# Kernel optimization log

Measured on AMD Instinct MI355X. Metric: run time of the kernel, lower is better.

The kernel has to match this reference:

```python
import jax, jax.numpy as jnp
from jax import lax
import numpy as np

FEAT_W = 52      # feature map width/height
IMG_W = 210      # input image width/height
SUB = IMG_W // FEAT_W  # = 4, sub_sample stride
N_ANCHOR = 9
NMS_THRESH = 0.7
PRE_NMS = 12000
POST_NMS = 2000
MIN_SIZE = 16.0


def make_anchors():
    # Faithful vectorization of generateAnchors: outer loop over ctr_x, inner over ctr_y,
    # then c unpacked as (ctr_y, ctr_x) = (x_val, y_val); ratios outer, scales inner.
    vals = (np.arange(SUB, (FEAT_W + 1) * SUB, SUB) - SUB // 2).astype(np.float64)  # 2,6,...,210
    cy = np.repeat(vals, FEAT_W)   # outer loop value -> anchor ctr_y
    cx = np.tile(vals, FEAT_W)     # inner loop value -> anchor ctr_x
    ratios = np.array([0.5, 1.0, 2.0])
    scales = np.array([4.0, 8.0, 16.0])
    h = (SUB * scales[None, :] * np.sqrt(ratios[:, None])).reshape(-1)      # (9,)
    w = (SUB * scales[None, :] * np.sqrt(1.0 / ratios[:, None])).reshape(-1)
    a = np.stack([cy[:, None] - h / 2.0, cx[:, None] - w / 2.0,
                  cy[:, None] + h / 2.0, cx[:, None] + w / 2.0], axis=-1)   # (2704, 9, 4)
    return a.reshape(-1, 4).astype(np.float32)  # (24336, 4) as [y1,x1,y2,x2]

_ANCHORS = jnp.asarray(make_anchors())


def _conv(x, w, b):
    y = lax.conv_general_dilated(x, w, (1, 1), 'SAME',
                                 dimension_numbers=('NCHW', 'OIHW', 'NCHW'))
    return y + b[None, :, None, None]


def propose_regions(locs, obj):
    # locs: (1, 24336, 4); obj: (1, 24336)
    anc = _ANCHORS
    ah = anc[:, 2] - anc[:, 0]
    aw = anc[:, 3] - anc[:, 1]
    acy = anc[:, 0] + 0.5 * ah
    acx = anc[:, 1] + 0.5 * aw
    l = locs[0]
    s = obj[0]
    cy = l[:, 0] * ah + acy
    cx = l[:, 1] * aw + acx
    hh = jnp.exp(l[:, 2]) * ah
    ww = jnp.exp(l[:, 3]) * aw
    roi = jnp.stack([cy - 0.5 * hh, cx - 0.5 * ww,
                     cy + 0.5 * hh, cx + 0.5 * ww], axis=1)
    roi = jnp.clip(roi, 0.0, float(IMG_W))
    hs = roi[:, 2] - roi[:, 0]
    ws = roi[:, 3] - roi[:, 1]
    valid = (hs >= MIN_SIZE) & (ws >= MIN_SIZE)
    # min_size filter folded into score masking; invalid boxes start suppressed
    masked = jnp.where(valid, s, -jnp.inf)
    order = jnp.argsort(-masked)[:PRE_NMS]
    boxes = roi[order]          # (PRE_NMS, 4) sorted by descending score
    v = valid[order]
    sgb = lax.stop_gradient(boxes)
    areas = (sgb[:, 3] - sgb[:, 1] + 1.0) * (sgb[:, 2] - sgb[:, 0] + 1.0)
    idxs = jnp.arange(PRE_NMS)

    def body(supp, i):
        b = sgb[i]
        yy1 = jnp.maximum(b[0], sgb[:, 0])
        xx1 = jnp.maximum(b[1], sgb[:, 1])
        yy2 = jnp.minimum(b[2], sgb[:, 2])
        xx2 = jnp.minimum(b[3], sgb[:, 3])
        inter = jnp.maximum(0.0, xx2 - xx1 + 1.0) * jnp.maximum(0.0, yy2 - yy1 + 1.0)
        iou = inter / (areas[i] + areas - inter)
        new = supp | ((iou > NMS_THRESH) & (idxs > i))
        return jnp.where(supp[i], supp, new), None

    supp, _ = lax.scan(body, ~v, idxs)  # greedy sequential NMS, fixed length
    keep = ~supp
    rank = jnp.cumsum(keep.astype(jnp.int32)) - 1
    write = keep & (rank < POST_NMS)
    tgt = jnp.where(write, rank, POST_NMS)  # overflow/dropped rows go to scrap slot
    out = jnp.zeros((POST_NMS + 1, 4), boxes.dtype).at[tgt].set(
        jnp.where(write[:, None], boxes, 0.0))
    return out[:POST_NMS]  # (2000, 4), zero-padded


def _forward(x, conv1_w, conv1_b, reg_w, reg_b, cls_w, cls_b):
    h = _conv(x, conv1_w, conv1_b)        # (1,256,52,52), no activation (as in source)
    reg = _conv(h, reg_w, reg_b)          # (1,36,52,52)
    cls = _conv(h, cls_w, cls_b)          # (1,18,52,52)
    locs = jnp.transpose(reg, (0, 2, 3, 1)).reshape(1, -1, 4)          # (1,24336,4)
    cls_t = jnp.transpose(cls, (0, 2, 3, 1))                            # (1,52,52,18)
    obj = cls_t.reshape(1, FEAT_W, FEAT_W, N_ANCHOR, 2)[..., 1].reshape(1, -1)
    cls_scores = cls_t.reshape(1, -1, 2)                                # (1,24336,2)
    rois = propose_regions(locs, obj)
    return rois, locs, cls_scores, obj


def setup_inputs() -> dict:
    key = jax.random.key(0)
    ks = jax.random.split(key, 4)
    x = jax.random.normal(ks[0], (1, 256, FEAT_W, FEAT_W), jnp.float32)
    conv1_w = 0.01 * jax.random.normal(ks[1], (256, 256, 3, 3), jnp.float32)
    conv1_b = jnp.zeros((256,), jnp.float32)
    reg_w = 0.01 * jax.random.normal(ks[2], (N_ANCHOR * 4, 256, 1, 1), jnp.float32)
    reg_b = jnp.zeros((N_ANCHOR * 4,), jnp.float32)
    cls_w = 0.01 * jax.random.normal(ks[3], (N_ANCHOR * 2, 256, 1, 1), jnp.float32)
    cls_b = jnp.zeros((N_ANCHOR * 2,), jnp.float32)
    return {"x": x, "conv1_w": conv1_w, "conv1_b": conv1_b,
            "reg_w": reg_w, "reg_b": reg_b, "cls_w": cls_w, "cls_b": cls_b}


def reference(x, conv1_w, conv1_b, reg_w, reg_b, cls_w, cls_b):
    rois, locs, cls_scores, obj = _forward(x, conv1_w, conv1_b, reg_w, reg_b, cls_w, cls_b)
    return (rois, locs, cls_scores, obj, cls_scores)
```

## Files before the change

### kernel.cpp

```cpp
#include <hip/hip_runtime.h>

typedef unsigned long long u64;
typedef unsigned int u32;

#define FEAT 52
#define NPIX 2704
#define NANC 24336
#define PRE  12000
#define POST 2000
#define ROWW 192
#define PADW 54
#define PADS 2916

#define ROIS_OFF 0
#define LOCS_OFF 8000
#define CLS_OFF  105344
#define OBJ_OFF  154016
#define CLS2_OFF 178352

#define OFF_W64   0ull
#define OFF_H64   4718592ull
#define OFF_REG64 10256384ull
#define OFF_SC64  11035136ull
#define OFF_ROI64 11229824ull
#define OFF_KEYS  12008576ull
#define OFF_SBOX  12270720ull
#define OFF_SAREA 12663936ull
#define OFF_SUPP  12762240ull
#define OFF_MASK  12763776ull
#define OFF_XPAD  OFF_MASK
#define OFF_H64B  (OFF_MASK + 2985984ull)

__global__ __launch_bounds__(256) void k_prep(const float* __restrict__ x,
                                              float* __restrict__ xpad,
                                              const float* __restrict__ w,
                                              double* __restrict__ w64) {
    int b = blockIdx.x;
    if (b < 2916) {
        int t = b * 256 + threadIdx.x;
        int ci = t / PADS, pos = t % PADS;
        int iy = pos / PADW, ix = pos % PADW;
        float v = 0.f;
        if (iy >= 1 && iy <= 52 && ix >= 1 && ix <= 52)
            v = x[ci * NPIX + (iy - 1) * FEAT + (ix - 1)];
        xpad[t] = v;
    } else {
        int t = (b - 2916) * 256 + threadIdx.x;
        int j = t & 3;
        int r = t >> 2;
        int k = r % 9;
        int r2 = r / 9;
        int ci = r2 & 255;
        int g = r2 >> 8;
        w64[t] = (double)w[(((g * 4 + j) * 256) + ci) * 9 + k];
    }
}

__global__ __launch_bounds__(256) void k_conv3(const float* __restrict__ xpad,
                                               const double* __restrict__ w64,
                                               const float* __restrict__ b,
                                               double* __restrict__ h64,
                                               double* __restrict__ h64b) {
    const int p = blockIdx.x * 256 + threadIdx.x;
    const int o0 = blockIdx.y * 4;
    const int half = blockIdx.z;
    if (p >= NPIX) return;
    const int y = p / FEAT, xq = p % FEAT;
    double a0, a1, a2, a3;
    if (half == 0) {
        a0 = (double)b[o0+0]; a1 = (double)b[o0+1];
        a2 = (double)b[o0+2]; a3 = (double)b[o0+3];
    } else {
        a0 = a1 = a2 = a3 = 0.0;
    }
    const int c0 = half << 7;
    const float* xb = xpad + (size_t)c0 * PADS + y * PADW + xq;
    const double* wb = w64 + (size_t)blockIdx.y * 9216 + c0 * 36;
    #pragma unroll 2
    for (int ci = 0; ci < 128; ++ci) {
        float f0 = xb[0],   f1 = xb[1],   f2 = xb[2];
        float f3 = xb[54],  f4 = xb[55],  f5 = xb[56];
        float f6 = xb[108], f7 = xb[109], f8 = xb[110];
        double xv[9];
        xv[0]=(double)f0; xv[1]=(double)f1; xv[2]=(double)f2;
        xv[3]=(double)f3; xv[4]=(double)f4; xv[5]=(double)f5;
        xv[6]=(double)f6; xv[7]=(double)f7; xv[8]=(double)f8;
        const double* wr = wb + ci * 36;
        #pragma unroll
        for (int k = 0; k < 9; ++k) {
            a0 += xv[k] * wr[4*k+0];
            a1 += xv[k] * wr[4*k+1];
            a2 += xv[k] * wr[4*k+2];
            a3 += xv[k] * wr[4*k+3];
        }
        xb += PADS;
    }
    double* ho = (half == 0) ? h64 : h64b;
    ho[(o0+0)*NPIX + p] = a0;
    ho[(o0+1)*NPIX + p] = a1;
    ho[(o0+2)*NPIX + p] = a2;
    ho[(o0+3)*NPIX + p] = a3;
}

__global__ __launch_bounds__(64) void k_conv1(const double* __restrict__ h64,
                                              const double* __restrict__ h64b,
                                              const float* __restrict__ regw,
                                              const float* __restrict__ regb,
                                              const float* __restrict__ clsw,
                                              const float* __restrict__ clsb,
                                              float* __restrict__ out,
                                              double* __restrict__ reg64,
                                              double* __restrict__ score64) {
    const int g = blockIdx.y;
    const int p = blockIdx.x * 64 + threadIdx.x;
    if (p >= NPIX) return;
    const bool isreg = (g < 4);
    const float* wbase = isreg ? (regw + g * 9 * 256) : (clsw + (g - 4) * 9 * 256);
    const float* bbase = isreg ? (regb + g * 9)       : (clsb + (g - 4) * 9);
    double acc[9];
    #pragma unroll
    for (int j = 0; j < 9; ++j) acc[j] = (double)bbase[j];
    #pragma unroll 4
    for (int ci = 0; ci < 256; ++ci) {
        double h = h64[ci * NPIX + p] + h64b[ci * NPIX + p];
        #pragma unroll
        for (int j = 0; j < 9; ++j)
            acc[j] += h * (double)wbase[j * 256 + ci];
    }
    #pragma unroll
    for (int j = 0; j < 9; ++j) {
        int oc = g * 9 + j;
        float v = (float)acc[j];
        if (isreg) {
            out[LOCS_OFF + p*36 + oc] = v;
            reg64[p*36 + oc] = acc[j];
        } else {
            int c = oc - 36;
            out[CLS_OFF  + p*18 + c] = v;
            out[CLS2_OFF + p*18 + c] = v;
            if (c & 1) {
                out[OBJ_OFF + p*9 + (c >> 1)] = v;
                score64[p*9 + (c >> 1)] = acc[j];
            }
        }
    }
}

__global__ __launch_bounds__(256) void k_decode(const double* __restrict__ reg64,
                                                const double* __restrict__ score64,
                                                double* __restrict__ roi64,
                                                u64* __restrict__ keys) {
    int t = blockIdx.x * 256 + threadIdx.x;
    if (t >= NANC) { keys[t] = ~0ull; return; }
    int pos = t / 9, a = t % 9;
    int py = pos / FEAT, px = pos % FEAT;
    int ri = a / 3, si = a % 3;
    double rat = (ri == 0) ? 0.5 : (ri == 1 ? 1.0 : 2.0);
    double scl = (si == 0) ? 4.0 : (si == 1 ? 8.0 : 16.0);
    double hA = 4.0 * scl * sqrt(rat);
    double wA = 4.0 * scl * sqrt(1.0 / rat);
    double cy0 = 4.0 * py + 2.0, cx0 = 4.0 * px + 2.0;
    float y1f = (float)(cy0 - hA / 2.0), x1f = (float)(cx0 - wA / 2.0);
    float y2f = (float)(cy0 + hA / 2.0), x2f = (float)(cx0 + wA / 2.0);
    double ah = (double)y2f - (double)y1f, aw = (double)x2f - (double)x1f;
    double acy = (double)y1f + 0.5 * ah, acx = (double)x1f + 0.5 * aw;
    double l0 = reg64[4*t+0], l1 = reg64[4*t+1], l2 = reg64[4*t+2], l3 = reg64[4*t+3];
    double cy = l0 * ah + acy, cx = l1 * aw + acx;
    double hh = exp(l2) * ah,  ww = exp(l3) * aw;
    double r0 = fmin(fmax(cy - 0.5*hh, 0.0), 210.0);
    double r1 = fmin(fmax(cx - 0.5*ww, 0.0), 210.0);
    double r2 = fmin(fmax(cy + 0.5*hh, 0.0), 210.0);
    double r3 = fmin(fmax(cx + 0.5*ww, 0.0), 210.0);
    roi64[4*t+0] = r0; roi64[4*t+1] = r1; roi64[4*t+2] = r2; roi64[4*t+3] = r3;
    bool valid = (r2 - r0 >= 16.0) && (r3 - r1 >= 16.0);
    double m = valid ? score64[t] : -__builtin_huge_val();
    long long ll = __double_as_longlong(m);
    u64 u = (u64)ll;
    u64 mono = (ll < 0) ? ~u : (u ^ 0x8000000000000000ull);
    keys[t] = ((~mono) & 0xFFFFFFFFFFFF0000ull) | (u64)t;
}

__global__ __launch_bounds__(1024) void k_sortA(u64* __restrict__ keys) {
    __shared__ u64 s[8192];
    const int base = blockIdx.x * 8192;
    for (int t = threadIdx.x; t < 8192; t += 1024) s[t] = keys[base + t];
    __syncthreads();
    for (int k = 2; k <= 8192; k <<= 1) {
        for (int j = k >> 1; j > 0; j >>= 1) {
            for (int q = threadIdx.x; q < 4096; q += 1024) {
                int i = ((q & ~(j-1)) << 1) | (q & (j-1));
                int l = i | j;
                bool asc = (((base + i) & k) == 0);
                u64 A = s[i], B = s[l];
                bool sw = asc ? (A > B) : (A < B);
                if (sw) { s[i] = B; s[l] = A; }
            }
            __syncthreads();
        }
    }
    for (int t = threadIdx.x; t < 8192; t += 1024) keys[base + t] = s[t];
}

__global__ __launch_bounds__(1024) void k_sortB(u64* __restrict__ keys, int k) {
    __shared__ u64 s[8192];
    const int base = blockIdx.x * 8192;
    for (int t = threadIdx.x; t < 8192; t += 1024) s[t] = keys[base + t];
    __syncthreads();
    for (int j = 4096; j > 0; j >>= 1) {
        for (int q = threadIdx.x; q < 4096; q += 1024) {
            int i = ((q & ~(j-1)) << 1) | (q & (j-1));
            int l = i | j;
            bool asc = (((base + i) & k) == 0);
            u64 A = s[i], B = s[l];
            bool sw = asc ? (A > B) : (A < B);
            if (sw) { s[i] = B; s[l] = A; }
        }
        __syncthreads();
    }
    for (int t = threadIdx.x; t < 8192; t += 1024) keys[base + t] = s[t];
}

__global__ __launch_bounds__(256) void k_sortG(u64* __restrict__ keys, int k, int j) {
    int t = blockIdx.x * 256 + threadIdx.x;
    int i = ((t & ~(j-1)) << 1) | (t & (j-1));
    int l = i | j;
    bool asc = ((i & k) == 0);
    u64 A = keys[i], B = keys[l];
    bool sw = asc ? (A > B) : (A < B);
    if (sw) { keys[i] = B; keys[l] = A; }
}

__global__ __launch_bounds__(256) void k_gather(const u64* __restrict__ keys,
                                                const double* __restrict__ roi64,
                                                double* __restrict__ sbox,
                                                double* __restrict__ sarea,
                                                u64* __restrict__ suppinit) {
    int p = blockIdx.x * 256 + threadIdx.x;
    bool sup = true;
    if (p < PRE) {
        int idx = (int)(keys[p] & 0xFFFFull);
        double b0 = roi64[4*idx+0], b1 = roi64[4*idx+1];
        double b2 = roi64[4*idx+2], b3 = roi64[4*idx+3];
        sbox[4*p+0] = b0; sbox[4*p+1] = b1; sbox[4*p+2] = b2; sbox[4*p+3] = b3;
        sarea[p] = (b3 - b1 + 1.0) * (b2 - b0 + 1.0);
        sup = !((b2 - b0 >= 16.0) && (b3 - b1 >= 16.0));
    } else {
        sbox[4*p+0] = 0.0; sbox[4*p+1] = 0.0; sbox[4*p+2] = 0.0; sbox[4*p+3] = 0.0;
        sarea[p] = 1.0;
    }
    u64 ball = __ballot(sup);
    if ((threadIdx.x & 63) == 0) suppinit[p >> 6] = ball;
}

__global__ __launch_bounds__(256) void k_mask(const double* __restrict__ sbox,
                                              const double* __restrict__ sarea,
                                              u64* __restrict__ mask) {
    const int jt = blockIdx.x, it = blockIdx.y;
    const int ib = it * 64, jb0 = jt * 1024;
    if (jb0 + 1023 <= ib) {
        for (int t = threadIdx.x; t < 1024; t += 256) {
            int ti = t >> 4, w = t & 15;
            int i = ib + ti;
            if (i < PRE) mask[(size_t)i * ROWW + jt*16 + w] = 0ull;
        }
        return;
    }
    __shared__ double jbx[4112];
    __shared__ double jar[1040];
    for (int t = threadIdx.x; t < 4096; t += 256) jbx[t + (t >> 8)] = sbox[(size_t)jb0*4 + t];
    for (int t = threadIdx.x; t < 1024; t += 256) jar[t + (t >> 6)] = sarea[jb0 + t];
    __syncthreads();
    int ti = threadIdx.x >> 2;
    int i = ib + ti;
    if (i >= PRE) return;
    double iy1 = sbox[4*i+0], ix1 = sbox[4*i+1], iy2 = sbox[4*i+2], ix2 = sbox[4*i+3];
    double iar = sarea[i];
    for (int w = (threadIdx.x & 3); w < 16; w += 4) {
        const double* jb = &jbx[257 * w];
        const double* ja = &jar[65 * w];
        u64 bits = 0ull;
        int q0 = w * 64;
        for (int l = 0; l < 64; ++l) {
            double jy1 = jb[4*l+0], jx1 = jb[4*l+1], jy2 = jb[4*l+2], jx2 = jb[4*l+3];
            double yy1 = fmax(iy1, jy1), xx1 = fmax(ix1, jx1);
            double yy2 = fmin(iy2, jy2), xx2 = fmin(ix2, jx2);
            double iw = fmax(xx2 - xx1 + 1.0, 0.0);
            double ih = fmax(yy2 - yy1 + 1.0, 0.0);
            double inter = iw * ih;
            bool s = ((jb0 + q0 + l) > i) && (inter > 0.7 * (iar + ja[l] - inter));
            bits |= ((u64)s) << l;
        }
        mask[(size_t)i * ROWW + jt*16 + w] = bits;
    }
}

__device__ inline u64 rdl64(u64 v, int l) {
    u32 lo = (u32)__builtin_amdgcn_readlane((int)(u32)v, l);
    u32 hi = (u32)__builtin_amdgcn_readlane((int)(u32)(v >> 32), l);
    return ((u64)hi << 32) | (u64)lo;
}
#define RFL64(lo, hi) ( ((u64)(u32)__builtin_amdgcn_readfirstlane((int)(hi)) << 32) \
                      | (u64)(u32)__builtin_amdgcn_readfirstlane((int)(lo)) )

__global__ __launch_bounds__(512) void k_scan(const u64* __restrict__ mask,
                                              const u64* __restrict__ suppinit,
                                              const double* __restrict__ sbox,
                                              float* __restrict__ rois) {
    __shared__ u64 dbuf[2][4608];
    __shared__ u32 keptLDS[POST];
    __shared__ u32 supp8[2][16];
    __shared__ int rankS, doneS;
    const int tid = threadIdx.x;
    const u32* suppinit32 = (const u32*)suppinit;

    if (tid < 16)                 supp8[0][tid]      = suppinit32[tid];
    else if (tid < 32)            supp8[1][tid - 16] = suppinit32[tid];
    if (tid == 0) { rankS = 0; doneS = 0; }
    for (int q = tid; q < 4096; q += 512) {
        int r = q >> 3, w = q & 7;
        dbuf[0][r*9 + w] = (r < PRE) ? mask[(size_t)r * ROWW + w] : 0ull;
    }
    __syncthreads();

    int rank0 = 0;
    for (int c = 0; c < 24; ++c) {
        const int nc = c + 1;
        const int cb = c & 1, nb = nc & 1;
        if (tid < 64) {
            const int lane = tid;
            u64 i0 = RFL64(supp8[cb][0],  supp8[cb][1]);
            u64 i1 = RFL64(supp8[cb][2],  supp8[cb][3]);
            u64 i2 = RFL64(supp8[cb][4],  supp8[cb][5]);
            u64 i3 = RFL64(supp8[cb][6],  supp8[cb][7]);
            u64 i4 = RFL64(supp8[cb][8],  supp8[cb][9]);
            u64 i5 = RFL64(supp8[cb][10], supp8[cb][11]);
            u64 i6 = RFL64(supp8[cb][12], supp8[cb][13]);
            u64 i7 = RFL64(supp8[cb][14], supp8[cb][15]);
            u64 a0=0,a1=0,a2=0,a3=0,a4=0,a5=0,a6=0,a7=0;
            int rk = __builtin_amdgcn_readfirstlane(rankS);
            bool dn = false;
#define GROUP(G)                                                                \
            if (!dn) {                                                          \
                u64 z = ~(i##G | a##G);                                         \
                if (z) {                                                        \
                    u64 r0=0,r1=0,r2=0,r3=0,r4=0,r5=0,r6=0,r7=0;                \
                    if ((z >> lane) & 1ull) {                                   \
                        const u64* rowp = &dbuf[cb][(G*64 + lane)*9];           \
                        r0=rowp[0]; r1=rowp[1]; r2=rowp[2]; r3=rowp[3];         \
                        r4=rowp[4]; r5=rowp[5]; r6=rowp[6]; r7=rowp[7];         \
                    }                                                           \
                    u64 keptm = 0;                                              \
                    while (z) {                                                 \
                        int bpos = (int)__builtin_ctzll(z);                     \
                        u64 q0=rdl64(r0,bpos), q1=rdl64(r1,bpos);               \
                        u64 q2=rdl64(r2,bpos), q3=rdl64(r3,bpos);               \
                        u64 q4=rdl64(r4,bpos), q5=rdl64(r5,bpos);               \
                        u64 q6=rdl64(r6,bpos), q7=rdl64(r7,bpos);               \
                        keptm |= (1ull << bpos);                                \
                        z &= ~(1ull << bpos) & ~q##G;                           \
                        a0|=q0; a1|=q1; a2|=q2; a3|=q3;                         \
                        a4|=q4; a5|=q5; a6|=q6; a7|=q7;                         \
                    }                                                           \
                    int pc = __builtin_popcountll(keptm);                       \
                    int navail = POST - rk;                                     \
                    int mylot = __builtin_amdgcn_mbcnt_hi((u32)(keptm >> 32),   \
                                 __builtin_amdgcn_mbcnt_lo((u32)keptm, 0));     \
                    if (((keptm >> lane) & 1) && mylot < navail)                \
                        keptLDS[rk + mylot] = (u32)(c*512 + G*64 + lane);       \
                    if (pc >= navail) { rk = POST; dn = true; }                 \
                    else rk += pc;                                              \
                }                                                               \
            }
            GROUP(0) GROUP(1) GROUP(2) GROUP(3)
            GROUP(4) GROUP(5) GROUP(6) GROUP(7)
#undef GROUP
            if (lane == 0) { rankS = rk; if (dn) doneS = 1; }
        } else if (tid < 256) {
            if (nc < 24) {
                for (int q = tid - 64; q < 4096; q += 192) {
                    int r = q >> 3, w = q & 7;
                    int i = nc*512 + r;
                    dbuf[nb][r*9 + w] = (i < PRE) ? mask[(size_t)i * ROWW + nc*8 + w] : 0ull;
                }
            }
        } else {
            if (nc < 24 && rank0 > 0) {
                u64 acc[8] = {0,0,0,0,0,0,0,0};
                for (int k = tid - 256; k < rank0; k += 256) {
                    const u64* rp = mask + (size_t)keptLDS[k] * ROWW + nc*8;
                    #pragma unroll
                    for (int w = 0; w < 8; ++w) acc[w] |= rp[w];
                }
                #pragma unroll
                for (int w = 0; w < 8; ++w) {
                    u64 v = acc[w];
                    #pragma unroll
                    for (int s = 1; s < 64; s <<= 1)
                        v |= (u64)__shfl_xor((unsigned long long)v, s, 64);
                    if ((tid & 63) == 0) {
                        if ((u32)v)         atomicOr(&supp8[nb][2*w],   (u32)v);
                        if ((u32)(v >> 32)) atomicOr(&supp8[nb][2*w+1], (u32)(v >> 32));
                    }
                }
            }
        }
        __syncthreads();
        if (doneS) break;
        if (nc >= 24) break;
        const int rk1 = rankS;
        {
            int w = tid & 7;
            u64 acc = 0;
            for (int k = rank0 + (tid >> 3); k < rk1; k += 64)
                acc |= mask[(size_t)keptLDS[k] * ROWW + nc*8 + w];
            if ((u32)acc)         atomicOr(&supp8[nb][2*w],   (u32)acc);
            if ((u32)(acc >> 32)) atomicOr(&supp8[nb][2*w+1], (u32)(acc >> 32));
            if (tid < 16) supp8[cb][tid] = (c + 2 < 24) ? suppinit32[(c+2)*16 + tid] : 0u;
        }
        rank0 = rk1;
        __syncthreads();
    }
    __syncthreads();
    const int R = rankS;
    for (int r = tid; r < POST; r += 512) {
        if (r < R) {
            int p = (int)keptLDS[r];
            rois[4*r+0] = (float)sbox[4*p+0];
            rois[4*r+1] = (float)sbox[4*p+1];
            rois[4*r+2] = (float)sbox[4*p+2];
            rois[4*r+3] = (float)sbox[4*p+3];
        }
    }
}

extern "C" void kernel_launch(void* const* d_in, const int* in_sizes, int n_in,
                              void* d_out, int out_size, void* d_ws, size_t ws_size,
                              hipStream_t stream) {
    const float* x    = (const float*)d_in[0];
    const float* w1   = (const float*)d_in[1];
    const float* b1   = (const float*)d_in[2];
    const float* regw = (const float*)d_in[3];
    const float* regb = (const float*)d_in[4];
    const float* clsw = (const float*)d_in[5];
    const float* clsb = (const float*)d_in[6];
    float* out = (float*)d_out;

    char* ws = (char*)d_ws;
    double* w64    = (double*)(ws + OFF_W64);
    double* h64    = (double*)(ws + OFF_H64);
    double* reg64  = (double*)(ws + OFF_REG64);
    double* sc64   = (double*)(ws + OFF_SC64);
    double* roi64  = (double*)(ws + OFF_ROI64);
    u64*    keys   = (u64*)   (ws + OFF_KEYS);
    double* sbox   = (double*)(ws + OFF_SBOX);
    double* sarea  = (double*)(ws + OFF_SAREA);
    u64*    supp0  = (u64*)   (ws + OFF_SUPP);
    u64*    maskp  = (u64*)   (ws + OFF_MASK);
    float*  xpad   = (float*) (ws + OFF_XPAD);
    double* h64b   = (double*)(ws + OFF_H64B);

    (void)hipMemsetAsync(d_out, 0, 8000 * sizeof(float), stream);

    k_prep<<<5220, 256, 0, stream>>>(x, xpad, w1, w64);
    k_conv3<<<dim3(11, 64, 2), 256, 0, stream>>>(xpad, w64, b1, h64, h64b);
    k_conv1<<<dim3(43, 6), 64, 0, stream>>>(h64, h64b, regw, regb, clsw, clsb, out, reg64, sc64);
    k_decode<<<128, 256, 0, stream>>>(reg64, sc64, roi64, keys);

    k_sortA<<<4, 1024, 0, stream>>>(keys);
    k_sortG<<<64, 256, 0, stream>>>(keys, 16384, 8192);
    k_sortB<<<4, 1024, 0, stream>>>(keys, 16384);
    k_sortG<<<64, 256, 0, stream>>>(keys, 32768, 16384);
    k_sortG<<<64, 256, 0, stream>>>(keys, 32768, 8192);
    k_sortB<<<4, 1024, 0, stream>>>(keys, 32768);

    k_gather<<<48, 256, 0, stream>>>(keys, roi64, sbox, sarea, supp0);
    k_mask<<<dim3(12, 188), 256, 0, stream>>>(sbox, sarea, maskp);
    k_scan<<<1, 512, 0, stream>>>(maskp, supp0, sbox, out + ROIS_OFF);
}
```

Measured before the change: 590.5 us.

## Store NMS mask chunks bit-transposed in LDS and scan with ballots

The serial NMS scan wave now keeps a per-lane suppression bit vector. Each 512-row mask chunk is bit-transposed (64x64 transpose through xor shuffles) before it is written to LDS. The greedy loop then uses ballots over a per-lane flag instead of eight 64-bit readlanes per kept box, which shortens the serial critical path. In exchange, every chunk load pays for a shuffle-based transpose, and the helper waves are reorganised so all seven non-scan waves both prefetch/transpose and OR kept rows.

```diff
diff --git a/kernel.cpp b/kernel.cpp
--- a/kernel.cpp
+++ b/kernel.cpp
@@ -294,31 +294,55 @@
     }
 }
 
-__device__ inline u64 rdl64(u64 v, int l) {
-    u32 lo = (u32)__builtin_amdgcn_readlane((int)(u32)v, l);
-    u32 hi = (u32)__builtin_amdgcn_readlane((int)(u32)(v >> 32), l);
-    return ((u64)hi << 32) | (u64)lo;
-}
-#define RFL64(lo, hi) ( ((u64)(u32)__builtin_amdgcn_readfirstlane((int)(hi)) << 32) \
-                      | (u64)(u32)__builtin_amdgcn_readfirstlane((int)(lo)) )
+__device__ inline u64 shflx64(u64 v, int m) {
+    int lo = __shfl_xor((int)(u32)v, m, 64);
+    int hi = __shfl_xor((int)(u32)(v >> 32), m, 64);
+    return ((u64)(u32)hi << 32) | (u64)(u32)lo;
+}
+__device__ inline u64 bitT64(u64 x, int lane) {
+#define TS(d, Mlo) { u64 y = shflx64(x, d); \
+    x = (lane & d) ? ((x & ~(Mlo)) | ((y >> d) & (Mlo))) \
+                   : ((x & (Mlo))  | ((y & (Mlo)) << d)); }
+    TS(32, 0x00000000FFFFFFFFull)
+    TS(16, 0x0000FFFF0000FFFFull)
+    TS(8,  0x00FF00FF00FF00FFull)
+    TS(4,  0x0F0F0F0F0F0F0F0Full)
+    TS(2,  0x3333333333333333ull)
+    TS(1,  0x5555555555555555ull)
+#undef TS
+    return x;
+}
 
 __global__ __launch_bounds__(512) void k_scan(const u64* __restrict__ mask,
                                               const u64* __restrict__ suppinit,
                                               const double* __restrict__ sbox,
                                               float* __restrict__ rois) {
-    __shared__ u64 dbuf[2][4608];
+    __shared__ u64 dbufT[2][4096];
     __shared__ u32 keptLDS[POST];
     __shared__ u32 supp8[2][16];
     __shared__ int rankS, doneS;
     const int tid = threadIdx.x;
     const u32* suppinit32 = (const u32*)suppinit;
 
-    if (tid < 16)                 supp8[0][tid]      = suppinit32[tid];
-    else if (tid < 32)            supp8[1][tid - 16] = suppinit32[tid];
+    if (tid < 16)      supp8[0][tid]      = suppinit32[tid];
+    else if (tid < 32) supp8[1][tid - 16] = suppinit32[tid];
     if (tid == 0) { rankS = 0; doneS = 0; }
-    for (int q = tid; q < 4096; q += 512) {
-        int r = q >> 3, w = q & 7;
-        dbuf[0][r*9 + w] = (r < PRE) ? mask[(size_t)r * ROWW + w] : 0ull;
+    {
+        const int w = tid >> 6, lane = tid & 63;
+        const int g = w;
+        int row = g*64 + lane;
+        u64 rw[8];
+        if (row < PRE) {
+            const u64* rp = mask + (size_t)row * ROWW;
+            #pragma unroll
+            for (int h = 0; h < 8; ++h) rw[h] = rp[h];
+        } else {
+            #pragma unroll
+            for (int h = 0; h < 8; ++h) rw[h] = 0ull;
+        }
+        #pragma unroll
+        for (int h = 0; h < 8; ++h)
+            dbufT[0][(g*8 + h)*64 + lane] = bitT64(rw[h], lane);
     }
     __syncthreads();
 
@@ -328,78 +352,73 @@
         const int cb = c & 1, nb = nc & 1;
         if (tid < 64) {
             const int lane = tid;
-            u64 i0 = RFL64(supp8[cb][0],  supp8[cb][1]);
-            u64 i1 = RFL64(supp8[cb][2],  supp8[cb][3]);
-            u64 i2 = RFL64(supp8[cb][4],  supp8[cb][5]);
-            u64 i3 = RFL64(supp8[cb][6],  supp8[cb][7]);
-            u64 i4 = RFL64(supp8[cb][8],  supp8[cb][9]);
-            u64 i5 = RFL64(supp8[cb][10], supp8[cb][11]);
-            u64 i6 = RFL64(supp8[cb][12], supp8[cb][13]);
-            u64 i7 = RFL64(supp8[cb][14], supp8[cb][15]);
-            u64 a0=0,a1=0,a2=0,a3=0,a4=0,a5=0,a6=0,a7=0;
-            int rk = __builtin_amdgcn_readfirstlane(rankS);
+            u32 sup = 0;
+            #pragma unroll
+            for (int h = 0; h < 8; ++h)
+                sup |= ((supp8[cb][2*h + (lane >> 5)] >> (lane & 31)) & 1u) << h;
+            int rk = rankS;
             bool dn = false;
-#define GROUP(G)                                                                \
-            if (!dn) {                                                          \
-                u64 z = ~(i##G | a##G);                                         \
-                if (z) {                                                        \
-                    u64 r0=0,r1=0,r2=0,r3=0,r4=0,r5=0,r6=0,r7=0;                \
-                    if ((z >> lane) & 1ull) {                                   \
-                        const u64* rowp = &dbuf[cb][(G*64 + lane)*9];           \
-                        r0=rowp[0]; r1=rowp[1]; r2=rowp[2]; r3=rowp[3];         \
-                        r4=rowp[4]; r5=rowp[5]; r6=rowp[6]; r7=rowp[7];         \
-                    }                                                           \
-                    u64 keptm = 0;                                              \
-                    while (z) {                                                 \
-                        int bpos = (int)__builtin_ctzll(z);                     \
-                        u64 q0=rdl64(r0,bpos), q1=rdl64(r1,bpos);               \
-                        u64 q2=rdl64(r2,bpos), q3=rdl64(r3,bpos);               \
-                        u64 q4=rdl64(r4,bpos), q5=rdl64(r5,bpos);               \
-                        u64 q6=rdl64(r6,bpos), q7=rdl64(r7,bpos);               \
-                        keptm |= (1ull << bpos);                                \
-                        z &= ~(1ull << bpos) & ~q##G;                           \
-                        a0|=q0; a1|=q1; a2|=q2; a3|=q3;                         \
-                        a4|=q4; a5|=q5; a6|=q6; a7|=q7;                         \
-                    }                                                           \
-                    int pc = __builtin_popcountll(keptm);                       \
-                    int navail = POST - rk;                                     \
-                    int mylot = __builtin_amdgcn_mbcnt_hi((u32)(keptm >> 32),   \
-                                 __builtin_amdgcn_mbcnt_lo((u32)keptm, 0));     \
-                    if (((keptm >> lane) & 1) && mylot < navail)                \
-                        keptLDS[rk + mylot] = (u32)(c*512 + G*64 + lane);       \
-                    if (pc >= navail) { rk = POST; dn = true; }                 \
-                    else rk += pc;                                              \
-                }                                                               \
+            for (int g = 0; g < 8; ++g) {
+                bool agj = !((sup >> g) & 1u);
+                u64 z = __ballot(agj);
+                if (!z) continue;
+                u64 tg[8];
+                #pragma unroll
+                for (int h = 0; h < 8; ++h) tg[h] = dbufT[cb][(g*8 + h)*64 + lane];
+                u64 keptm = 0;
+                while (z) {
+                    int i = (int)__builtin_ctzll(z);
+                    keptm |= (1ull << i);
+                    agj = agj && !((tg[g] >> i) & 1ull);
+                    u64 m2 = (i < 63) ? (~0ull << (i + 1)) : 0ull;
+                    z = __ballot(agj) & m2;
+                }
+                int pc = __builtin_popcountll(keptm);
+                int navail = POST - rk;
+                int mylot = __builtin_amdgcn_mbcnt_hi((u32)(keptm >> 32),
+                             __builtin_amdgcn_mbcnt_lo((u32)keptm, 0));
+                if (((keptm >> lane) & 1) && mylot < navail)
+                    keptLDS[rk + mylot] = (u32)(c*512 + g*64 + lane);
+                if (pc >= navail) { rk = POST; dn = true; break; }
+                rk += pc;
+                #pragma unroll
+                for (int h = 0; h < 8; ++h)
+                    if (h > g && (tg[h] & keptm)) sup |= (1u << h);
             }
-            GROUP(0) GROUP(1) GROUP(2) GROUP(3)
-            GROUP(4) GROUP(5) GROUP(6) GROUP(7)
-#undef GROUP
             if (lane == 0) { rankS = rk; if (dn) doneS = 1; }
-        } else if (tid < 256) {
-            if (nc < 24) {
-                for (int q = tid - 64; q < 4096; q += 192) {
-                    int r = q >> 3, w = q & 7;
-                    int i = nc*512 + r;
-                    dbuf[nb][r*9 + w] = (i < PRE) ? mask[(size_t)i * ROWW + nc*8 + w] : 0ull;
+        } else if (nc < 24) {
+            const int w = tid >> 6, lane = tid & 63;
+            for (int g = w - 1; g < 8; g += 7) {
+                int row = nc*512 + g*64 + lane;
+                u64 rw[8];
+                if (row < PRE) {
+                    const u64* rp = mask + (size_t)row * ROWW + nc*8;
+                    #pragma unroll
+                    for (int h = 0; h < 8; ++h) rw[h] = rp[h];
+                } else {
+                    #pragma unroll
+                    for (int h = 0; h < 8; ++h) rw[h] = 0ull;
                 }
+                #pragma unroll
+                for (int h = 0; h < 8; ++h)
+                    dbufT[nb][(g*8 + h)*64 + lane] = bitT64(rw[h], lane);
             }
-        } else {
-            if (nc < 24 && rank0 > 0) {
+            if (rank0 > 0) {
                 u64 acc[8] = {0,0,0,0,0,0,0,0};
-                for (int k = tid - 256; k < rank0; k += 256) {
+                for (int k = tid - 64; k < rank0; k += 448) {
                     const u64* rp = mask + (size_t)keptLDS[k] * ROWW + nc*8;
                     #pragma unroll
-                    for (int w = 0; w < 8; ++w) acc[w] |= rp[w];
+                    for (int h2 = 0; h2 < 8; ++h2) acc[h2] |= rp[h2];
                 }
                 #pragma unroll
-                for (int w = 0; w < 8; ++w) {
-                    u64 v = acc[w];
+                for (int h2 = 0; h2 < 8; ++h2) {
+                    u64 v = acc[h2];
                     #pragma unroll
                     for (int s = 1; s < 64; s <<= 1)
                         v |= (u64)__shfl_xor((unsigned long long)v, s, 64);
-                    if ((tid & 63) == 0) {
-                        if ((u32)v)         atomicOr(&supp8[nb][2*w],   (u32)v);
-                        if ((u32)(v >> 32)) atomicOr(&supp8[nb][2*w+1], (u32)(v >> 32));
+                    if (lane == 0) {
+                        if ((u32)v)         atomicOr(&supp8[nb][2*h2],   (u32)v);
+                        if ((u32)(v >> 32)) atomicOr(&supp8[nb][2*h2+1], (u32)(v >> 32));
                     }
                 }
             }
```

After: 556.0 us. 5.8% less time.
